# Performance work log

Measured on AMD Instinct MI355X. Metric: run time of the kernel, lower is better.

## Reference

```python
import jax, jax.numpy as jnp
import numpy as np

N, D = 8192, 128

def _rbf_kernel(x, y):
    # InfoVAE-style kernel: exp(-mean((x_i - y_j)^2) / dim) = exp(-sqdist / dim^2)
    dim = x.shape[1]
    x2 = jnp.sum(x * x, axis=1)              # [n]
    y2 = jnp.sum(y * y, axis=1)              # [m]
    sqdist = x2[:, None] + y2[None, :] - 2.0 * (x @ y.T)  # [n, m]
    return jnp.exp(-sqdist / (dim * dim))


def setup_inputs() -> dict:
    key = jax.random.key(0)
    k1, k2 = jax.random.split(key)
    inputs = jax.random.normal(k1, (N, D), dtype=jnp.float32)
    true_samples = jax.random.normal(k2, (N, D), dtype=jnp.float32)
    return {"inputs": inputs, "true_samples": true_samples}


def reference(inputs, true_samples):
    x = true_samples  # samples from standard normal prior
    y = inputs
    k_xx = _rbf_kernel(x, x)
    k_yy = _rbf_kernel(y, y)
    k_xy = _rbf_kernel(x, y)
    mmd = jnp.mean(k_xx) + jnp.mean(k_yy) - 2.0 * jnp.mean(k_xy)
    return mmd
```

## Files before the change

kernel.cpp:

```cpp
#include <hip/hip_runtime.h>
#include <hip/hip_bf16.h>
#include <math.h>


#define NN 8192
#define DD 128
#define TZ 16384
#define SPLIT 12
#define NBLK (64 * SPLIT)

typedef __attribute__((ext_vector_type(8))) short bf16x8;
typedef __attribute__((ext_vector_type(4))) float f32x4;
typedef __attribute__((ext_vector_type(2))) float f32x2;

#if __has_builtin(__builtin_amdgcn_exp2f)
#define EXP2F __builtin_amdgcn_exp2f
#else
#define EXP2F exp2f
#endif

constexpr float LOG2E = 0x1.715476p+0f;
constexpr float S2 = LOG2E / 8192.0f;

constexpr size_t PLANE = 1048576;

#define LDS_B 32768
#define LDS_NORM 49152
#define LDS_RED 50176

constexpr size_t WS_NORM = 2048;
constexpr size_t WS_Z    = WS_NORM + (size_t)TZ * sizeof(float);

__device__ __forceinline__ void gload_lds16(const void* g, void* l) {
  __builtin_amdgcn_global_load_lds(
      (const __attribute__((address_space(1))) void*)g,
      (__attribute__((address_space(3))) void*)l, 16, 0, 0);
}

__global__ __launch_bounds__(256) void prep(
    const float* __restrict__ X, const float* __restrict__ Y,
    char* __restrict__ Zs, float* __restrict__ normZ,
    double* __restrict__ sums) {
  if (blockIdx.x == 0) sums[threadIdx.x] = 0.0;

  const int row = blockIdx.x * 4 + (threadIdx.x >> 6);
  const int lane = threadIdx.x & 63;
  const float* __restrict__ src =
      (row < NN) ? (X + (size_t)row * DD) : (Y + (size_t)(row - NN) * DD);
  const float2 v = *reinterpret_cast<const float2*>(src + 2 * lane);

  float n = v.x * v.x + v.y * v.y;

  const int ks = lane >> 4;
  const int quadc = (lane >> 2) & 3;
  const int inner = (lane & 3) * 4;
  char* dst = Zs + (size_t)ks * PLANE + (size_t)row * 64 +
              ((quadc ^ ((row >> 1) & 3)) << 4) + inner;
  *reinterpret_cast<__hip_bfloat162*>(dst) =
      __hip_bfloat162{__float2bfloat16(v.x), __float2bfloat16(v.y)};

#pragma unroll
  for (int o = 32; o > 0; o >>= 1) n += __shfl_down(n, o);
  if (lane == 0) normZ[row] = n * (-LOG2E / 16384.0f);
}

__global__ __launch_bounds__(256, 3) void mmd_mfma(
    const char* __restrict__ Zs, const float* __restrict__ normZ,
    double* __restrict__ sums) {
  __shared__ alignas(16) char lds[50176 + 64];

  const int bid = blockIdx.x;
  const int p = bid / SPLIT, s = bid % SPLIT;
  const int q = 127 - p;
  const int n1 = (127 - p - s) / 12 + 1;
  const int u0 = s + 12 * n1 - (128 - p);
  const int n2 = (u0 <= p) ? (p - u0) / 12 + 1 : 0;

  const int segI[2]  = {p, q};
  const int segJ0[2] = {p + s, q + u0};
  const int segN[2]  = {n1, n2};

  const int tid = threadIdx.x;
  const int lane = tid & 63, wave = tid >> 6;
  const int wr = wave >> 1, wc = wave & 1;
  const int lr = lane & 15, quad = lane >> 4;

  char* ldwA = lds + wave * 2048;

  const int csw = (quad ^ ((lr >> 1) & 3)) << 4;
  const char* aRd = lds + (wr * 64 + lr) * 64 + csw;
  const char* bRd = lds + LDS_B + (wc * 64 + lr) * 64 + csw;

  bf16x8 a[4], b[4];
  f32x4 ar[4];

#define STAGE_B(base, sl, buf) do {                                         \
    gload_lds16((base) + (size_t)(sl) * PLANE,                              \
                lds + LDS_B + (buf) * 8192 + wave * 2048);                  \
    gload_lds16((base) + (size_t)(sl) * PLANE + 1024,                       \
                lds + LDS_B + (buf) * 8192 + wave * 2048 + 1024);           \
  } while (0)

#define LOADFRAGS(ks, buf) do {                                             \
    _Pragma("unroll")                                                       \
    for (int i = 0; i < 4; ++i)                                             \
      a[i] = *reinterpret_cast<const bf16x8*>(aRd + (ks) * 8192 + i * 1024);\
    _Pragma("unroll")                                                       \
    for (int j = 0; j < 4; ++j)                                             \
      b[j] = *reinterpret_cast<const bf16x8*>(bRd + (buf) * 8192 + j * 1024);\
  } while (0)

#define MFMAS() do {                                                        \
    __builtin_amdgcn_s_setprio(1);                                          \
    _Pragma("unroll")                                                       \
    for (int i = 0; i < 4; ++i)                                             \
      _Pragma("unroll")                                                     \
      for (int j = 0; j < 4; ++j)                                           \
        acc[i][j] = __builtin_amdgcn_mfma_f32_16x16x32_bf16(                \
            a[i], b[j], acc[i][j], 0, 0, 0);                                \
    __builtin_amdgcn_s_setprio(0);                                          \
  } while (0)

  const f32x2 s2v = {S2, S2};
  double blockAcc = 0.0;

  for (int seg = 0; seg < 2; ++seg) {
    const int I = segI[seg];
    const int nIter = segN[seg];
    if (nIter == 0) continue;
    int J = segJ0[seg];

    const float* nzA = normZ + I * 128 + wr * 64;
#pragma unroll
    for (int i = 0; i < 4; ++i)
      ar[i] = *reinterpret_cast<const f32x4*>(nzA + i * 16 + quad * 4);

    const char* srcA0 = Zs + (size_t)(I * 128 + wave * 32) * 64 + lane * 16;
#pragma unroll
    for (int ks = 0; ks < 4; ++ks) {
      gload_lds16(srcA0 + (size_t)ks * PLANE,        ldwA + ks * 8192);
      gload_lds16(srcA0 + (size_t)ks * PLANE + 1024, ldwA + ks * 8192 + 1024);
    }

    const char* srcB = Zs + (size_t)(J * 128 + wave * 32) * 64 + lane * 16;
    const char* normB = (const char*)normZ + (size_t)J * 512 + lane * 16;

    STAGE_B(srcB, 0, 0);
    STAGE_B(srcB, 1, 1);
    asm volatile("s_waitcnt vmcnt(0)\n\ts_barrier" ::: "memory");

    for (int it = 0; it < nIter; ++it) {
      const char* srcBn = (it + 1 < nIter) ? srcB + SPLIT * 8192 : srcB;
      f32x4 acc[4][4] = {};

      asm volatile("s_waitcnt vmcnt(2)\n\ts_barrier" ::: "memory");
      LOADFRAGS(0, 0);
      asm volatile("s_waitcnt lgkmcnt(0)\n\ts_barrier" ::: "memory");
      __builtin_amdgcn_sched_barrier(0);
      STAGE_B(srcB, 2, 0);
      gload_lds16(normB, lds + LDS_NORM);
      __builtin_amdgcn_sched_barrier(0);
      MFMAS();

      asm volatile("s_waitcnt vmcnt(3)\n\ts_barrier" ::: "memory");
      LOADFRAGS(1, 1);
      asm volatile("s_waitcnt lgkmcnt(0)\n\ts_barrier" ::: "memory");
      __builtin_amdgcn_sched_barrier(0);
      STAGE_B(srcB, 3, 1);
      __builtin_amdgcn_sched_barrier(0);
      MFMAS();

      asm volatile("s_waitcnt vmcnt(3)\n\ts_barrier" ::: "memory");
      LOADFRAGS(2, 0);
      asm volatile("s_waitcnt lgkmcnt(0)\n\ts_barrier" ::: "memory");
      __builtin_amdgcn_sched_barrier(0);
      STAGE_B(srcBn, 0, 0);
      __builtin_amdgcn_sched_barrier(0);
      MFMAS();

      asm volatile("s_waitcnt vmcnt(2)\n\ts_barrier" ::: "memory");
      LOADFRAGS(3, 1);
      asm volatile("s_waitcnt lgkmcnt(0)\n\ts_barrier" ::: "memory");
      __builtin_amdgcn_sched_barrier(0);
      STAGE_B(srcBn, 1, 1);
      __builtin_amdgcn_sched_barrier(0);
      MFMAS();

      float cb[4];
#pragma unroll
      for (int j = 0; j < 4; ++j)
        cb[j] = *reinterpret_cast<const float*>(
            lds + LDS_NORM + (wc * 64 + j * 16 + lr) * 4);

      f32x2 part01 = {0.f, 0.f}, part23 = {0.f, 0.f};
#pragma unroll
      for (int i = 0; i < 4; ++i) {
        const f32x2 ar01 = {ar[i].x, ar[i].y};
        const f32x2 ar23 = {ar[i].z, ar[i].w};
#pragma unroll
        for (int j = 0; j < 4; ++j) {
          const f32x2 rb2 = {cb[j], cb[j]};
          const f32x2 base01 = ar01 + rb2;
          const f32x2 base23 = ar23 + rb2;
          const f32x2 acc01 = {acc[i][j][0], acc[i][j][1]};
          const f32x2 acc23 = {acc[i][j][2], acc[i][j][3]};
          const f32x2 arg01 = __builtin_elementwise_fma(acc01, s2v, base01);
          const f32x2 arg23 = __builtin_elementwise_fma(acc23, s2v, base23);
          part01 += (f32x2){EXP2F(arg01.x), EXP2F(arg01.y)};
          part23 += (f32x2){EXP2F(arg23.x), EXP2F(arg23.y)};
        }
      }
      const f32x2 ps = part01 + part23;
      double w = ((I < 64) == (J < 64)) ? 1.0 : -1.0;
      if (I != J) w += w;
      blockAcc += (double)(ps.x + ps.y) * w;

      J += SPLIT;
      srcB += SPLIT * 8192;
      normB += SPLIT * 512;
    }

    asm volatile("s_waitcnt vmcnt(0)\n\ts_barrier" ::: "memory");
  }

#undef STAGE_B
#undef LOADFRAGS
#undef MFMAS

#pragma unroll
  for (int o = 32; o > 0; o >>= 1) blockAcc += __shfl_down(blockAcc, o);
  double* red = reinterpret_cast<double*>(lds + LDS_RED);
  if (lane == 0) red[wave] = blockAcc;
  __syncthreads();
  if (tid == 0)
    atomicAdd(&sums[bid & 255], red[0] + red[1] + red[2] + red[3]);
}

__global__ void finish(const double* __restrict__ s, float* __restrict__ out) {
  double v = s[threadIdx.x] + s[threadIdx.x + 64] + s[threadIdx.x + 128] +
             s[threadIdx.x + 192];
#pragma unroll
  for (int o = 32; o > 0; o >>= 1) v += __shfl_down(v, o);
  if (threadIdx.x == 0)
    out[0] = (float)(v * (1.0 / ((double)NN * (double)NN)));
}

extern "C" void kernel_launch(void* const* d_in, const int* in_sizes, int n_in,
                              void* d_out, int out_size, void* d_ws, size_t ws_size,
                              hipStream_t stream) {
  const float* y_inputs = (const float*)d_in[0];
  const float* x_true   = (const float*)d_in[1];
  float* out = (float*)d_out;

  char* ws = (char*)d_ws;
  double* sums = (double*)ws;
  float* normZ = (float*)(ws + WS_NORM);
  char* Zs = ws + WS_Z;

  prep<<<TZ / 4, 256, 0, stream>>>(x_true, y_inputs, Zs, normZ, sums);
  mmd_mfma<<<NBLK, 256, 0, stream>>>(Zs, normZ, sums);
  finish<<<1, 64, 0, stream>>>(sums, out);
}
```

Baseline: 102.0 us.

## Load B fragments directly from global into registers, dropping LDS staging

B-tile fragments now go straight from global memory (pre-swizzled bf16 planes) into a double-buffered register set instead of being staged through LDS, and the per-iteration barriers are removed. Column norms are also read directly from global memory instead of through LDS. The LDS footprint shrinks to only the A tile, which may allow more resident blocks. The cost is that global-load latency is exposed inside the MFMA loop with only one K-slice of prefetch, and the loads are 16-byte-per-lane accesses that are less coalesced.

```diff
diff --git a/kernel.cpp b/kernel.cpp
--- a/kernel.cpp
+++ b/kernel.cpp
@@ -24,9 +24,7 @@
 
 constexpr size_t PLANE = 1048576;
 
-#define LDS_B 32768
-#define LDS_NORM 49152
-#define LDS_RED 50176
+#define LDS_RED 32768
 
 constexpr size_t WS_NORM = 2048;
 constexpr size_t WS_Z    = WS_NORM + (size_t)TZ * sizeof(float);
@@ -67,14 +65,14 @@
 __global__ __launch_bounds__(256, 3) void mmd_mfma(
     const char* __restrict__ Zs, const float* __restrict__ normZ,
     double* __restrict__ sums) {
-  __shared__ alignas(16) char lds[50176 + 64];
+  __shared__ alignas(16) char lds[LDS_RED + 64];
 
   const int bid = blockIdx.x;
   const int p = bid / SPLIT, s = bid % SPLIT;
   const int q = 127 - p;
-  const int n1 = (127 - p - s) / 12 + 1;
-  const int u0 = s + 12 * n1 - (128 - p);
-  const int n2 = (u0 <= p) ? (p - u0) / 12 + 1 : 0;
+  const int n1 = (127 - p - s) / SPLIT + 1;
+  const int u0 = s + SPLIT * n1 - (128 - p);
+  const int n2 = (u0 <= p) ? (p - u0) / SPLIT + 1 : 0;
 
   const int segI[2]  = {p, q};
   const int segJ0[2] = {p + s, q + u0};
@@ -85,39 +83,34 @@
   const int wr = wave >> 1, wc = wave & 1;
   const int lr = lane & 15, quad = lane >> 4;
 
-  char* ldwA = lds + wave * 2048;
-
   const int csw = (quad ^ ((lr >> 1) & 3)) << 4;
   const char* aRd = lds + (wr * 64 + lr) * 64 + csw;
-  const char* bRd = lds + LDS_B + (wc * 64 + lr) * 64 + csw;
-
-  bf16x8 a[4], b[4];
+  const size_t bOff = (size_t)(wc * 64 + lr) * 64 + csw;
+
+  bf16x8 a[4], b0[4], b1[4];
   f32x4 ar[4];
 
-#define STAGE_B(base, sl, buf) do {                                         \
-    gload_lds16((base) + (size_t)(sl) * PLANE,                              \
-                lds + LDS_B + (buf) * 8192 + wave * 2048);                  \
-    gload_lds16((base) + (size_t)(sl) * PLANE + 1024,                       \
-                lds + LDS_B + (buf) * 8192 + wave * 2048 + 1024);           \
-  } while (0)
-
-#define LOADFRAGS(ks, buf) do {                                             \
+#define LOADA(ks) do {                                                      \
     _Pragma("unroll")                                                       \
     for (int i = 0; i < 4; ++i)                                             \
       a[i] = *reinterpret_cast<const bf16x8*>(aRd + (ks) * 8192 + i * 1024);\
+  } while (0)
+
+#define LOADB(dst, base, pl) do {                                           \
     _Pragma("unroll")                                                       \
     for (int j = 0; j < 4; ++j)                                             \
-      b[j] = *reinterpret_cast<const bf16x8*>(bRd + (buf) * 8192 + j * 1024);\
+      dst[j] = *reinterpret_cast<const bf16x8*>(                            \
+          (base) + (size_t)(pl) * PLANE + j * 1024);                        \
   } while (0)
 
-#define MFMAS() do {                                                        \
+#define MFMAS(bb) do {                                                      \
     __builtin_amdgcn_s_setprio(1);                                          \
     _Pragma("unroll")                                                       \
     for (int i = 0; i < 4; ++i)                                             \
       _Pragma("unroll")                                                     \
       for (int j = 0; j < 4; ++j)                                           \
         acc[i][j] = __builtin_amdgcn_mfma_f32_16x16x32_bf16(                \
-            a[i], b[j], acc[i][j], 0, 0, 0);                                \
+            a[i], bb[j], acc[i][j], 0, 0, 0);                               \
     __builtin_amdgcn_s_setprio(0);                                          \
   } while (0)
 
@@ -136,61 +129,45 @@
       ar[i] = *reinterpret_cast<const f32x4*>(nzA + i * 16 + quad * 4);
 
     const char* srcA0 = Zs + (size_t)(I * 128 + wave * 32) * 64 + lane * 16;
+    char* ldwA = lds + wave * 2048;
 #pragma unroll
     for (int ks = 0; ks < 4; ++ks) {
       gload_lds16(srcA0 + (size_t)ks * PLANE,        ldwA + ks * 8192);
       gload_lds16(srcA0 + (size_t)ks * PLANE + 1024, ldwA + ks * 8192 + 1024);
     }
 
-    const char* srcB = Zs + (size_t)(J * 128 + wave * 32) * 64 + lane * 16;
-    const char* normB = (const char*)normZ + (size_t)J * 512 + lane * 16;
-
-    STAGE_B(srcB, 0, 0);
-    STAGE_B(srcB, 1, 1);
+    const char* bbase = Zs + (size_t)J * 8192 + bOff;
+    LOADB(b0, bbase, 0);
     asm volatile("s_waitcnt vmcnt(0)\n\ts_barrier" ::: "memory");
 
     for (int it = 0; it < nIter; ++it) {
-      const char* srcBn = (it + 1 < nIter) ? srcB + SPLIT * 8192 : srcB;
+      const char* bnext = (it + 1 < nIter) ? bbase + SPLIT * 8192 : bbase;
       f32x4 acc[4][4] = {};
 
-      asm volatile("s_waitcnt vmcnt(2)\n\ts_barrier" ::: "memory");
-      LOADFRAGS(0, 0);
-      asm volatile("s_waitcnt lgkmcnt(0)\n\ts_barrier" ::: "memory");
-      __builtin_amdgcn_sched_barrier(0);
-      STAGE_B(srcB, 2, 0);
-      gload_lds16(normB, lds + LDS_NORM);
-      __builtin_amdgcn_sched_barrier(0);
-      MFMAS();
-
-      asm volatile("s_waitcnt vmcnt(3)\n\ts_barrier" ::: "memory");
-      LOADFRAGS(1, 1);
-      asm volatile("s_waitcnt lgkmcnt(0)\n\ts_barrier" ::: "memory");
-      __builtin_amdgcn_sched_barrier(0);
-      STAGE_B(srcB, 3, 1);
-      __builtin_amdgcn_sched_barrier(0);
-      MFMAS();
-
-      asm volatile("s_waitcnt vmcnt(3)\n\ts_barrier" ::: "memory");
-      LOADFRAGS(2, 0);
-      asm volatile("s_waitcnt lgkmcnt(0)\n\ts_barrier" ::: "memory");
-      __builtin_amdgcn_sched_barrier(0);
-      STAGE_B(srcBn, 0, 0);
-      __builtin_amdgcn_sched_barrier(0);
-      MFMAS();
-
-      asm volatile("s_waitcnt vmcnt(2)\n\ts_barrier" ::: "memory");
-      LOADFRAGS(3, 1);
-      asm volatile("s_waitcnt lgkmcnt(0)\n\ts_barrier" ::: "memory");
-      __builtin_amdgcn_sched_barrier(0);
-      STAGE_B(srcBn, 1, 1);
-      __builtin_amdgcn_sched_barrier(0);
-      MFMAS();
-
+      LOADB(b1, bbase, 1);
+      LOADA(0);
+      __builtin_amdgcn_sched_barrier(0);
+      MFMAS(b0);
+
+      LOADB(b0, bbase, 2);
+      LOADA(1);
+      __builtin_amdgcn_sched_barrier(0);
+      MFMAS(b1);
+
+      LOADB(b1, bbase, 3);
+      LOADA(2);
+      __builtin_amdgcn_sched_barrier(0);
+      MFMAS(b0);
+
+      LOADB(b0, bnext, 0);
+      LOADA(3);
+      __builtin_amdgcn_sched_barrier(0);
+      MFMAS(b1);
+
+      const float* nzB = normZ + J * 128 + wc * 64;
       float cb[4];
 #pragma unroll
-      for (int j = 0; j < 4; ++j)
-        cb[j] = *reinterpret_cast<const float*>(
-            lds + LDS_NORM + (wc * 64 + j * 16 + lr) * 4);
+      for (int j = 0; j < 4; ++j) cb[j] = nzB[j * 16 + lr];
 
       f32x2 part01 = {0.f, 0.f}, part23 = {0.f, 0.f};
 #pragma unroll
@@ -216,15 +193,14 @@
       blockAcc += (double)(ps.x + ps.y) * w;
 
       J += SPLIT;
-      srcB += SPLIT * 8192;
-      normB += SPLIT * 512;
+      bbase = bnext;
     }
 
-    asm volatile("s_waitcnt vmcnt(0)\n\ts_barrier" ::: "memory");
+    __syncthreads();
   }
 
-#undef STAGE_B
-#undef LOADFRAGS
+#undef LOADA
+#undef LOADB
 #undef MFMAS
 
 #pragma unroll
```

New measurement: 101.9 us, median of 2. No clear change (-0.2%).
